# Performance work log

Hardware: AMD Instinct MI355X
Metric: run time of the kernel (lower is better)

Reference implementation:

```python
import jax, jax.numpy as jnp
import numpy as np

N_HIDDEN_LAYERS = 9  # 32->32 middle layers (plus input 1->32 and output 32->1)
HID = 32
SLOPE = 0.01  # LeakyReLU negative_slope


def leaky_relu(x):
    return jnp.where(x >= 0, x, SLOPE * x)


def setup_inputs() -> dict:
    key = jax.random.key(0)
    ks = jax.random.split(key, 8)
    N = 1048576
    x = jax.random.normal(ks[0], (N,), dtype=jnp.float32)
    # PyTorch Linear init: U(-1/sqrt(fan_in), 1/sqrt(fan_in))
    def u(k, shape, fan_in):
        b = 1.0 / np.sqrt(fan_in)
        return jax.random.uniform(k, shape, jnp.float32, -b, b)
    W_in = u(ks[1], (1, HID), 1)
    b_in = u(ks[2], (HID,), 1)
    W_hid = u(ks[3], (N_HIDDEN_LAYERS, HID, HID), HID)
    b_hid = u(ks[4], (N_HIDDEN_LAYERS, HID), HID)
    W_out = u(ks[5], (HID, 1), HID)
    b_out = u(ks[6], (1,), HID)
    return {"x": x, "W_in": W_in, "b_in": b_in, "W_hid": W_hid,
            "b_hid": b_hid, "W_out": W_out, "b_out": b_out}


def reference(x, W_in, b_in, W_hid, b_hid, W_out, b_out):
    N = x.shape[0]
    h = x[:, None]  # [N, 1], mirrors x.reshape(N, 1)
    h = leaky_relu(h @ W_in + b_in)  # [N, 32]
    def step(h, wb):
        W, b = wb
        return leaky_relu(h @ W + b), None
    h, _ = jax.lax.scan(step, h, (W_hid, b_hid))
    out = h @ W_out + b_out  # [N, 1]
    return out.reshape(1, N)
```

## Files before the change

kernel.cpp:

```cpp
#include <hip/hip_runtime.h>

#define NLAYERS 9
#define HID 32
#define SLOPE 0.01f

typedef _Float16 v2h __attribute__((ext_vector_type(2)));
typedef _Float16 v8h __attribute__((ext_vector_type(8)));
typedef float v16f __attribute__((ext_vector_type(16)));

#define NCHAIN 4

union U8 { v8h v; v2h p[4]; };
struct B4 { v2h a, b, c, d; };

__device__ __forceinline__ v2h pk_cvt(float a, float b) {
    return __builtin_bit_cast(v2h, __builtin_amdgcn_cvt_pkrtz(a, b));
}
__device__ __forceinline__ v2h leaky2(v2h t, v2h s) {
    return __builtin_elementwise_max(t, t * s);
}
__device__ __forceinline__ int qmap(int k) {
    int c = k >> 4, h = (k >> 3) & 1, t = k & 7;
    return 16 * c + 4 * h + (t & 3) + 8 * (t >> 2);
}
__device__ __forceinline__ int rmap(int reg, int h) {
    return (reg & 3) + 8 * (reg >> 2) + 4 * h;
}

__global__ __launch_bounds__(256, 2) void mlp_mfma_kernel(
    const float* __restrict__ x,
    const float* __restrict__ W_in,
    const float* __restrict__ b_in,
    const float* __restrict__ W_hid,
    const float* __restrict__ b_hid,
    const float* __restrict__ W_out,
    const float* __restrict__ b_out,
    float* __restrict__ out, int N)
{
    __shared__ __align__(16) v2h bias_sh[NLAYERS][2][8];
    for (int t = threadIdx.x; t < NLAYERS * 16; t += blockDim.x) {
        int l = t >> 4, r = t & 15, h = r >> 3, j = r & 7;
        bias_sh[l][h][j] = v2h{(_Float16)b_hid[l * HID + rmap(2 * j, h)],
                               (_Float16)b_hid[l * HID + rmap(2 * j + 1, h)]};
    }
    __syncthreads();

    const int lane = threadIdx.x & 63;
    const int half = lane >> 5;
    const int m    = lane & 31;

    v8h alo[NLAYERS], ahi[NLAYERS];
#pragma unroll
    for (int l = 0; l < NLAYERS; ++l) {
        const float* Wl = W_hid + l * HID * HID;
#pragma unroll
        for (int j = 0; j < 8; ++j) {
            alo[l][j] = (_Float16)Wl[qmap(8 * half + j) * HID + m];
            ahi[l][j] = (_Float16)Wl[qmap(16 + 8 * half + j) * HID + m];
        }
    }
    v2h win2[8], bin2[8], wout2[8];
#pragma unroll
    for (int u = 0; u < 8; ++u) {
        int i0 = 2 * u, i1 = 2 * u + 1;
        int d0 = qmap(((i0 >> 3) << 4) + 8 * half + (i0 & 7));
        int d1 = qmap(((i1 >> 3) << 4) + 8 * half + (i1 & 7));
        win2[u]  = v2h{(_Float16)W_in[d0],  (_Float16)W_in[d1]};
        bin2[u]  = v2h{(_Float16)b_in[d0],  (_Float16)b_in[d1]};
        wout2[u] = v2h{(_Float16)W_out[d0], (_Float16)W_out[d1]};
    }
    const float bo = b_out[0];
    const v2h slope2 = v2h{(_Float16)SLOPE, (_Float16)SLOPE};
    const v16f z16 = {};

    const int nwaves = (gridDim.x * blockDim.x) >> 6;
    const int wid    = (blockIdx.x * blockDim.x + threadIdx.x) >> 6;
    const int niter  = (N + NCHAIN * 32 - 1) / (NCHAIN * 32);

    float xc[NCHAIN] = {0.0f, 0.0f, 0.0f, 0.0f};
    if (wid < niter) {
#pragma unroll
        for (int c = 0; c < NCHAIN; ++c) {
            int idx = wid * (NCHAIN * 32) + c * 32 + m;
            xc[c] = (idx < N) ? x[idx] : 0.0f;
        }
    }

    for (int it = wid; it < niter; it += nwaves) {
        float xn[NCHAIN] = {0.0f, 0.0f, 0.0f, 0.0f};
        {
            int nit = it + nwaves;
            if (nit < niter) {
#pragma unroll
                for (int c = 0; c < NCHAIN; ++c) {
                    int idx = nit * (NCHAIN * 32) + c * 32 + m;
                    xn[c] = (idx < N) ? x[idx] : 0.0f;
                }
            }
        }

        U8 clo[NCHAIN], chi[NCHAIN];
#pragma unroll
        for (int c = 0; c < NCHAIN; ++c) {
            _Float16 xh = (_Float16)xc[c];
            v2h x2 = v2h{xh, xh};
#pragma unroll
            for (int u = 0; u < 4; ++u) {
                clo[c].p[u] = leaky2(x2 * win2[u] + bin2[u], slope2);
                chi[c].p[u] = leaky2(x2 * win2[4 + u] + bin2[4 + u], slope2);
            }
        }

#pragma unroll
        for (int l = 0; l < NLAYERS; ++l) {
            B4 q0 = __builtin_bit_cast(B4, ((const uint4*)&bias_sh[l][half][0])[0]);
            B4 q1 = __builtin_bit_cast(B4, ((const uint4*)&bias_sh[l][half][4])[0]);

            v16f a[NCHAIN];
#pragma unroll
            for (int c = 0; c < NCHAIN; ++c)
                a[c] = __builtin_amdgcn_mfma_f32_32x32x16_f16(alo[l], clo[c].v, z16, 0, 0, 0);
#pragma unroll
            for (int c = 0; c < NCHAIN; ++c)
                a[c] = __builtin_amdgcn_mfma_f32_32x32x16_f16(ahi[l], chi[c].v, a[c], 0, 0, 0);

            v2h bl[8] = {q0.a, q0.b, q0.c, q0.d, q1.a, q1.b, q1.c, q1.d};
#pragma unroll
            for (int c = 0; c < NCHAIN; ++c) {
#pragma unroll
                for (int u = 0; u < 4; ++u) {
                    clo[c].p[u] = leaky2(pk_cvt(a[c][2 * u], a[c][2 * u + 1]) + bl[u], slope2);
                    chi[c].p[u] = leaky2(pk_cvt(a[c][8 + 2 * u], a[c][8 + 2 * u + 1]) + bl[4 + u], slope2);
                }
            }
        }

#pragma unroll
        for (int c = 0; c < NCHAIN; ++c) {
            float p = 0.0f;
#pragma unroll
            for (int u = 0; u < 4; ++u) {
                p = fmaf((float)clo[c].p[u][0], (float)wout2[u][0], p);
                p = fmaf((float)clo[c].p[u][1], (float)wout2[u][1], p);
                p = fmaf((float)chi[c].p[u][0], (float)wout2[4 + u][0], p);
                p = fmaf((float)chi[c].p[u][1], (float)wout2[4 + u][1], p);
            }
            float o = p + __shfl_xor(p, 32, 64) + bo;
            int idx = it * (NCHAIN * 32) + c * 32 + m;
            if (half == (c >> 1) && idx < N) out[idx] = o;
        }

#pragma unroll
        for (int c = 0; c < NCHAIN; ++c) xc[c] = xn[c];
    }
}

extern "C" void kernel_launch(void* const* d_in, const int* in_sizes, int n_in,
                              void* d_out, int out_size, void* d_ws, size_t ws_size,
                              hipStream_t stream) {
    const float* x     = (const float*)d_in[0];
    const float* W_in  = (const float*)d_in[1];
    const float* b_in  = (const float*)d_in[2];
    const float* W_hid = (const float*)d_in[3];
    const float* b_hid = (const float*)d_in[4];
    const float* W_out = (const float*)d_in[5];
    const float* b_out = (const float*)d_in[6];
    float* out = (float*)d_out;

    int N = in_sizes[0];
    dim3 block(256);
    dim3 grid(512);
    mlp_mfma_kernel<<<grid, block, 0, stream>>>(x, W_in, b_in, W_hid, b_hid,
                                                W_out, b_out, out, N);
}
```

Measured before the change: 96.15 us.

## Switch hidden layers to 16x16x32 MFMA with 8 independent sample chains

Replaces the 32x32x16 MFMA formulation, which needed two chained MFMAs per layer, with the 16x16x32 f16 MFMA. Each layer now runs two independent MFMAs per chain covering the two 16-row output halves, and the weight, bias and activation register layouts are remapped so MFMA outputs feed the next layer's B operand directly. Chains per wave go from 4 to 8 with 16 samples each, which removes the dependent accumulate between MFMAs and adds independent work to hide latency. The output reduction now needs two cross-lane shuffles instead of one.

```diff
diff --git a/kernel.cpp b/kernel.cpp
--- a/kernel.cpp
+++ b/kernel.cpp
@@ -3,28 +3,19 @@
 #define NLAYERS 9
 #define HID 32
 #define SLOPE 0.01f
+#define NCHAIN 8
 
 typedef _Float16 v2h __attribute__((ext_vector_type(2)));
 typedef _Float16 v8h __attribute__((ext_vector_type(8)));
-typedef float v16f __attribute__((ext_vector_type(16)));
-
-#define NCHAIN 4
+typedef float v4f __attribute__((ext_vector_type(4)));
 
 union U8 { v8h v; v2h p[4]; };
-struct B4 { v2h a, b, c, d; };
 
 __device__ __forceinline__ v2h pk_cvt(float a, float b) {
     return __builtin_bit_cast(v2h, __builtin_amdgcn_cvt_pkrtz(a, b));
 }
 __device__ __forceinline__ v2h leaky2(v2h t, v2h s) {
     return __builtin_elementwise_max(t, t * s);
-}
-__device__ __forceinline__ int qmap(int k) {
-    int c = k >> 4, h = (k >> 3) & 1, t = k & 7;
-    return 16 * c + 4 * h + (t & 3) + 8 * (t >> 2);
-}
-__device__ __forceinline__ int rmap(int reg, int h) {
-    return (reg & 3) + 8 * (reg >> 2) + 4 * h;
 }
 
 __global__ __launch_bounds__(256, 2) void mlp_mfma_kernel(
@@ -37,121 +28,110 @@
     const float* __restrict__ b_out,
     float* __restrict__ out, int N)
 {
-    __shared__ __align__(16) v2h bias_sh[NLAYERS][2][8];
+    __shared__ __align__(16) v2h bias_sh[NLAYERS][4][4];
     for (int t = threadIdx.x; t < NLAYERS * 16; t += blockDim.x) {
-        int l = t >> 4, r = t & 15, h = r >> 3, j = r & 7;
-        bias_sh[l][h][j] = v2h{(_Float16)b_hid[l * HID + rmap(2 * j, h)],
-                               (_Float16)b_hid[l * HID + rmap(2 * j + 1, h)]};
+        int l = t >> 4, r = t & 15, g = r >> 2, j2 = r & 3;
+        bias_sh[l][g][j2] = v2h{(_Float16)b_hid[l * HID + 8 * g + 2 * j2],
+                                (_Float16)b_hid[l * HID + 8 * g + 2 * j2 + 1]};
     }
     __syncthreads();
 
     const int lane = threadIdx.x & 63;
-    const int half = lane >> 5;
-    const int m    = lane & 31;
+    const int g    = lane >> 4;
+    const int c    = lane & 15;
 
-    v8h alo[NLAYERS], ahi[NLAYERS];
+    const int outbase = 8 * (c >> 2) + (c & 3);
+    v8h aW[NLAYERS][2];
 #pragma unroll
     for (int l = 0; l < NLAYERS; ++l) {
         const float* Wl = W_hid + l * HID * HID;
 #pragma unroll
-        for (int j = 0; j < 8; ++j) {
-            alo[l][j] = (_Float16)Wl[qmap(8 * half + j) * HID + m];
-            ahi[l][j] = (_Float16)Wl[qmap(16 + 8 * half + j) * HID + m];
-        }
+        for (int a = 0; a < 2; ++a)
+#pragma unroll
+            for (int j = 0; j < 8; ++j)
+                aW[l][a][j] = (_Float16)Wl[(8 * g + j) * HID + outbase + 4 * a];
     }
-    v2h win2[8], bin2[8], wout2[8];
+    v2h win2[4], bin2[4], wout2[4];
 #pragma unroll
-    for (int u = 0; u < 8; ++u) {
-        int i0 = 2 * u, i1 = 2 * u + 1;
-        int d0 = qmap(((i0 >> 3) << 4) + 8 * half + (i0 & 7));
-        int d1 = qmap(((i1 >> 3) << 4) + 8 * half + (i1 & 7));
-        win2[u]  = v2h{(_Float16)W_in[d0],  (_Float16)W_in[d1]};
-        bin2[u]  = v2h{(_Float16)b_in[d0],  (_Float16)b_in[d1]};
-        wout2[u] = v2h{(_Float16)W_out[d0], (_Float16)W_out[d1]};
+    for (int u = 0; u < 4; ++u) {
+        int d = 8 * g + 2 * u;
+        win2[u]  = v2h{(_Float16)W_in[d],  (_Float16)W_in[d + 1]};
+        bin2[u]  = v2h{(_Float16)b_in[d],  (_Float16)b_in[d + 1]};
+        wout2[u] = v2h{(_Float16)W_out[d], (_Float16)W_out[d + 1]};
     }
     const float bo = b_out[0];
     const v2h slope2 = v2h{(_Float16)SLOPE, (_Float16)SLOPE};
-    const v16f z16 = {};
+    const v4f z4 = {};
 
     const int nwaves = (gridDim.x * blockDim.x) >> 6;
     const int wid    = (blockIdx.x * blockDim.x + threadIdx.x) >> 6;
-    const int niter  = (N + NCHAIN * 32 - 1) / (NCHAIN * 32);
+    const int niter  = (N + NCHAIN * 16 - 1) / (NCHAIN * 16);
 
-    float xc[NCHAIN] = {0.0f, 0.0f, 0.0f, 0.0f};
-    if (wid < niter) {
+    float xc[NCHAIN];
 #pragma unroll
-        for (int c = 0; c < NCHAIN; ++c) {
-            int idx = wid * (NCHAIN * 32) + c * 32 + m;
-            xc[c] = (idx < N) ? x[idx] : 0.0f;
-        }
+    for (int ch = 0; ch < NCHAIN; ++ch) {
+        int idx = wid * (NCHAIN * 16) + ch * 16 + c;
+        xc[ch] = (idx < N) ? x[idx] : 0.0f;
     }
 
     for (int it = wid; it < niter; it += nwaves) {
-        float xn[NCHAIN] = {0.0f, 0.0f, 0.0f, 0.0f};
+        float xn[NCHAIN];
         {
             int nit = it + nwaves;
-            if (nit < niter) {
 #pragma unroll
-                for (int c = 0; c < NCHAIN; ++c) {
-                    int idx = nit * (NCHAIN * 32) + c * 32 + m;
-                    xn[c] = (idx < N) ? x[idx] : 0.0f;
-                }
+            for (int ch = 0; ch < NCHAIN; ++ch) {
+                int idx = nit * (NCHAIN * 16) + ch * 16 + c;
+                xn[ch] = (nit < niter && idx < N) ? x[idx] : 0.0f;
             }
         }
 
-        U8 clo[NCHAIN], chi[NCHAIN];
+        U8 hb[NCHAIN];
 #pragma unroll
-        for (int c = 0; c < NCHAIN; ++c) {
-            _Float16 xh = (_Float16)xc[c];
+        for (int ch = 0; ch < NCHAIN; ++ch) {
+            _Float16 xh = (_Float16)xc[ch];
             v2h x2 = v2h{xh, xh};
 #pragma unroll
-            for (int u = 0; u < 4; ++u) {
-                clo[c].p[u] = leaky2(x2 * win2[u] + bin2[u], slope2);
-                chi[c].p[u] = leaky2(x2 * win2[4 + u] + bin2[4 + u], slope2);
+            for (int u = 0; u < 4; ++u)
+                hb[ch].p[u] = leaky2(x2 * win2[u] + bin2[u], slope2);
+        }
+
+#pragma unroll
+        for (int l = 0; l < NLAYERS; ++l) {
+            v2h bl0 = bias_sh[l][g][0], bl1 = bias_sh[l][g][1];
+            v2h bl2 = bias_sh[l][g][2], bl3 = bias_sh[l][g][3];
+
+            v4f a0[NCHAIN], a1[NCHAIN];
+#pragma unroll
+            for (int ch = 0; ch < NCHAIN; ++ch) {
+                a0[ch] = __builtin_amdgcn_mfma_f32_16x16x32_f16(aW[l][0], hb[ch].v, z4, 0, 0, 0);
+                a1[ch] = __builtin_amdgcn_mfma_f32_16x16x32_f16(aW[l][1], hb[ch].v, z4, 0, 0, 0);
+            }
+#pragma unroll
+            for (int ch = 0; ch < NCHAIN; ++ch) {
+                hb[ch].p[0] = leaky2(pk_cvt(a0[ch][0], a0[ch][1]) + bl0, slope2);
+                hb[ch].p[1] = leaky2(pk_cvt(a0[ch][2], a0[ch][3]) + bl1, slope2);
+                hb[ch].p[2] = leaky2(pk_cvt(a1[ch][0], a1[ch][1]) + bl2, slope2);
+                hb[ch].p[3] = leaky2(pk_cvt(a1[ch][2], a1[ch][3]) + bl3, slope2);
             }
         }
 
 #pragma unroll
-        for (int l = 0; l < NLAYERS; ++l) {
-            B4 q0 = __builtin_bit_cast(B4, ((const uint4*)&bias_sh[l][half][0])[0]);
-            B4 q1 = __builtin_bit_cast(B4, ((const uint4*)&bias_sh[l][half][4])[0]);
-
-            v16f a[NCHAIN];
+        for (int ch = 0; ch < NCHAIN; ++ch) {
+            float p = 0.0f;
 #pragma unroll
-            for (int c = 0; c < NCHAIN; ++c)
-                a[c] = __builtin_amdgcn_mfma_f32_32x32x16_f16(alo[l], clo[c].v, z16, 0, 0, 0);
-#pragma unroll
-            for (int c = 0; c < NCHAIN; ++c)
-                a[c] = __builtin_amdgcn_mfma_f32_32x32x16_f16(ahi[l], chi[c].v, a[c], 0, 0, 0);
-
-            v2h bl[8] = {q0.a, q0.b, q0.c, q0.d, q1.a, q1.b, q1.c, q1.d};
-#pragma unroll
-            for (int c = 0; c < NCHAIN; ++c) {
-#pragma unroll
-                for (int u = 0; u < 4; ++u) {
-                    clo[c].p[u] = leaky2(pk_cvt(a[c][2 * u], a[c][2 * u + 1]) + bl[u], slope2);
-                    chi[c].p[u] = leaky2(pk_cvt(a[c][8 + 2 * u], a[c][8 + 2 * u + 1]) + bl[4 + u], slope2);
-                }
+            for (int u = 0; u < 4; ++u) {
+                p = fmaf((float)hb[ch].p[u][0], (float)wout2[u][0], p);
+                p = fmaf((float)hb[ch].p[u][1], (float)wout2[u][1], p);
             }
+            p += __shfl_xor(p, 16, 64);
+            p += __shfl_xor(p, 32, 64);
+            float o = p + bo;
+            int idx = it * (NCHAIN * 16) + ch * 16 + c;
+            if (g == (ch & 3) && idx < N) out[idx] = o;
         }
 
 #pragma unroll
-        for (int c = 0; c < NCHAIN; ++c) {
-            float p = 0.0f;
-#pragma unroll
-            for (int u = 0; u < 4; ++u) {
-                p = fmaf((float)clo[c].p[u][0], (float)wout2[u][0], p);
-                p = fmaf((float)clo[c].p[u][1], (float)wout2[u][1], p);
-                p = fmaf((float)chi[c].p[u][0], (float)wout2[4 + u][0], p);
-                p = fmaf((float)chi[c].p[u][1], (float)wout2[4 + u][1], p);
-            }
-            float o = p + __shfl_xor(p, 32, 64) + bo;
-            int idx = it * (NCHAIN * 32) + c * 32 + m;
-            if (half == (c >> 1) && idx < N) out[idx] = o;
-        }
-
-#pragma unroll
-        for (int c = 0; c < NCHAIN; ++c) xc[c] = xn[c];
+        for (int ch = 0; ch < NCHAIN; ++ch) xc[ch] = xn[ch];
     }
 }
 
```

New measurement: 96.64 us. Within noise of the previous version (+0.5%).
